# Optimization experiments

Hardware: AMD Instinct MI355X
Metric: run time of the kernel (lower is better)

The kernel has to match this reference:

```python
import jax, jax.numpy as jnp
import numpy as np

DELTA_PULL = 0.5
DELTA_PUSH = 1.5
EPS = 1e-6


def setup_inputs() -> dict:
    key = jax.random.key(0)
    k1, k2 = jax.random.split(key)
    B, C, H, W, K = 4, 16, 512, 512, 16
    embedding_maps = jax.random.normal(k1, (B, C, H, W), dtype=jnp.float32)
    instance_masks = jax.random.randint(k2, (B, K, H, W), 0, 2, dtype=jnp.int32)
    return {"embedding_maps": embedding_maps, "instance_masks": instance_masks}


def reference(embedding_maps, instance_masks):
    emb = embedding_maps                      # [B, C, H, W]
    m = (instance_masks > 0).astype(emb.dtype)  # [B, K, H, W]
    K = m.shape[1]

    # per-instance masked segment reductions over all H*W pixels
    counts = m.sum((-1, -2))                                   # [B, K]
    sums = jnp.einsum('bchw,bkhw->bkc', emb, m)                # [B, K, C]
    sq_sums = jnp.einsum('bchw,bkhw->bkc', emb * emb, m)       # [B, K, C]

    valid = counts > 0                                          # [B, K]
    safe_counts = jnp.maximum(counts, 1.0)
    means = sums / safe_counts[..., None]                       # [B, K, C] exact fg mean

    # sum over fg pixels of ||e - mean||^2 = sq_sum - 2*mean.sum + n*mean^2
    pull_k = (sq_sums - 2.0 * means * sums + counts[..., None] * means * means).sum(-1)
    pull_k = jnp.where(valid, pull_k / (counts + EPS), 0.0)     # [B, K]

    M = valid.sum(-1).astype(emb.dtype)                         # [B] num valid instances
    pull_b = pull_k.sum(-1) / jnp.maximum(M, 1.0)               # [B]

    # pairwise push between valid instance means (i < j)
    diff = means[:, :, None, :] - means[:, None, :, :]          # [B, K, K, C]
    dist = jnp.sqrt((diff * diff).sum(-1) + 1e-12)              # [B, K, K]
    iu = jnp.arange(K)
    pair = valid[:, :, None] & valid[:, None, :] & (iu[:, None] < iu[None, :])
    push_terms = jnp.where(pair, jnp.maximum(DELTA_PUSH - dist, 0.0) ** 2, 0.0)
    npairs = M * (M - 1.0) / 2.0
    push_b = jnp.where(M > 1.0, push_terms.sum((-1, -2)) / jnp.maximum(npairs, 1.0), 0.0)

    return (DELTA_PULL * pull_b + push_b).mean()
```

## Files before the change

### kernel.cpp

```cpp
#include <hip/hip_runtime.h>

#define BB 4
#define CC 16
#define KK 16
#define HWP (512 * 512)
#define THREADS 512
#define TPW 128
#define TPB ((THREADS / 64) * TPW)
#define NTILES (HWP / TPB)
#define NGROUP (TPW / 32)
#define NWAVE (THREADS / 64)
#define NSLICE 16
#define WSTOT (64 + 1024 + 1024)

typedef short bf16x8 __attribute__((ext_vector_type(8)));
typedef float f32x4 __attribute__((ext_vector_type(4)));

__device__ __forceinline__ float fmaxf_(float a, float b) { return a > b ? a : b; }

__device__ __forceinline__ unsigned short f2bf(float f) {
    unsigned u = __float_as_uint(f);
    u += 0x7FFFu + ((u >> 16) & 1u);
    return (unsigned short)(u >> 16);
}
__device__ __forceinline__ unsigned pkbf(float x, float y) {
    return (unsigned)f2bf(x) | ((unsigned)f2bf(y) << 16);
}

__global__ __launch_bounds__(THREADS, 8) void disc_mfma_kernel(
    const float* __restrict__ emb, const int* __restrict__ masks,
    float* __restrict__ ws)
{
    __shared__ __align__(16) unsigned short bits[TPB];
    __shared__ float redbuf[NWAVE][64][9];
    __shared__ float cnt_red[NWAVE][16];

    const int tid = threadIdx.x;
    const int lane = tid & 63;
    const int wave = tid >> 6;
    const int b = blockIdx.x / NTILES;
    const int tile = blockIdx.x % NTILES;
    const size_t base_px = (size_t)tile * TPB + wave * TPW;

    const int quad = lane >> 4;
    const int r = lane & 15;

    const int* mbase = masks + (size_t)b * KK * HWP + base_px + 2 * lane;
    unsigned v0 = 0, v1 = 0;
    #pragma unroll
    for (int k = 0; k < KK; ++k) {
        int2 mm = *(const int2*)(mbase + (size_t)k * HWP);
        v0 |= (mm.x > 0 ? 1u : 0u) << k;
        v1 |= (mm.y > 0 ? 1u : 0u) << k;
    }
    ((unsigned*)bits)[wave * (TPW / 2) + lane] = v0 | (v1 << 16);

    union { bf16x8 v; unsigned short s[8]; } Bones;
    #pragma unroll
    for (int i = 0; i < 8; ++i) Bones.s[i] = 0x3F80;

    const float* ebase = emb + ((size_t)b * CC + r) * HWP + base_px;

    f32x4 acc_s = {0.f, 0.f, 0.f, 0.f};
    f32x4 acc_q = {0.f, 0.f, 0.f, 0.f};
    f32x4 acc_c = {0.f, 0.f, 0.f, 0.f};

    #pragma unroll
    for (int g = 0; g < NGROUP; ++g) {
        const int p0 = wave * TPW + g * 32;

        uint4 bw = *(const uint4*)&bits[p0 + quad * 8];
        union { bf16x8 v; unsigned u[4]; } A;
        A.u[0] = ((bw.x >> r) & 0x00010001u) * 0x3F80u;
        A.u[1] = ((bw.y >> r) & 0x00010001u) * 0x3F80u;
        A.u[2] = ((bw.z >> r) & 0x00010001u) * 0x3F80u;
        A.u[3] = ((bw.w >> r) & 0x00010001u) * 0x3F80u;

        const float4* ep = (const float4*)(ebase + g * 32 + quad * 8);
        float4 f0 = ep[0], f1 = ep[1];
        union { bf16x8 v; unsigned u[4]; } Bf, B2;
        Bf.u[0] = pkbf(f0.x, f0.y);
        Bf.u[1] = pkbf(f0.z, f0.w);
        Bf.u[2] = pkbf(f1.x, f1.y);
        Bf.u[3] = pkbf(f1.z, f1.w);
        B2.u[0] = pkbf(f0.x * f0.x, f0.y * f0.y);
        B2.u[1] = pkbf(f0.z * f0.z, f0.w * f0.w);
        B2.u[2] = pkbf(f1.x * f1.x, f1.y * f1.y);
        B2.u[3] = pkbf(f1.z * f1.z, f1.w * f1.w);

        acc_s = __builtin_amdgcn_mfma_f32_16x16x32_bf16(A.v, Bf.v, acc_s, 0, 0, 0);
        acc_q = __builtin_amdgcn_mfma_f32_16x16x32_bf16(A.v, B2.v, acc_q, 0, 0, 0);
        acc_c = __builtin_amdgcn_mfma_f32_16x16x32_bf16(A.v, Bones.v, acc_c, 0, 0, 0);
    }

    #pragma unroll
    for (int j = 0; j < 4; ++j) {
        redbuf[wave][lane][j] = acc_s[j];
        redbuf[wave][lane][4 + j] = acc_q[j];
    }
    if (r == 0) {
        #pragma unroll
        for (int reg = 0; reg < 4; ++reg) cnt_red[wave][quad * 4 + reg] = acc_c[reg];
    }
    __syncthreads();

    float* slice = ws + (size_t)(blockIdx.x & (NSLICE - 1)) * WSTOT;
    {
        const int fi = tid;
        const int l2 = fi >> 3, j = fi & 7;
        float v = 0.f;
        #pragma unroll
        for (int w = 0; w < NWAVE; ++w) v += redbuf[w][l2][j];
        const int reg = j & 3, isq = j >> 2;
        const int krow = (l2 >> 4) * 4 + reg;
        const int ccol = l2 & 15;
        atomicAdd(&slice[64 + isq * 1024 + ((size_t)b * KK + krow) * CC + ccol], v);
    }
    if (tid < KK) {
        float ctot = 0.f;
        #pragma unroll
        for (int w = 0; w < NWAVE; ++w) ctot += cnt_red[w][tid];
        atomicAdd(&slice[b * KK + tid], ctot);
    }
}

__global__ __launch_bounds__(1024) void disc_finalize_kernel(
    const float* __restrict__ ws, float* __restrict__ out)
{
    __shared__ float red[WSTOT];
    __shared__ float means[BB][KK][CC];
    __shared__ float partial[BB];
    const int tid = threadIdx.x;

    for (int i4 = tid; i4 < WSTOT / 4; i4 += 1024) {
        float4 t = {0.f, 0.f, 0.f, 0.f};
        #pragma unroll
        for (int s = 0; s < NSLICE; ++s) {
            float4 v = *(const float4*)(ws + (size_t)s * WSTOT + 4 * i4);
            t.x += v.x; t.y += v.y; t.z += v.z; t.w += v.w;
        }
        *(float4*)(red + 4 * i4) = t;
    }
    __syncthreads();

    const float* red_cnt = red;
    const float* red_sum = red + 64;
    const float* red_sq  = red + 64 + 1024;

    const int b = tid >> 6;
    const int lane = tid & 63;
    const bool active = tid < 256;

    const float DELTA_PULL = 0.5f;
    const float DELTA_PUSH = 1.5f;
    const float EPS = 1e-6f;

    unsigned long long bal = 0ull;
    float M = 0.f, pull_b = 0.f;

    if (active) {
        float cntk = 0.f;
        bool valid = false;
        float pull_k = 0.f;
        if (lane < KK) {
            int k = lane;
            cntk = red_cnt[b * KK + k];
            valid = cntk > 0.f;
            float safe = fmaxf_(cntk, 1.f);
            float acc_sq = 0.f, acc_ss = 0.f;
            #pragma unroll
            for (int c = 0; c < CC; ++c) {
                float sv = red_sum[(b * KK + k) * CC + c];
                means[b][k][c] = sv / safe;
                acc_sq += red_sq[(b * KK + k) * CC + c];
                acc_ss += sv * sv;
            }
            if (valid) pull_k = (acc_sq - acc_ss / cntk) / (cntk + EPS);
        }

        bal = __ballot(lane < KK && valid);
        M = (float)__popcll(bal);

        float ps = pull_k;
        #pragma unroll
        for (int d = 32; d >= 1; d >>= 1) ps += __shfl_xor(ps, d, 64);
        pull_b = ps / fmaxf_(M, 1.f);
    }

    __syncthreads();

    if (active) {
        float push = 0.f;
        for (int t = lane; t < KK * KK; t += 64) {
            int i = t >> 4, j = t & 15;
            if (i < j && ((bal >> i) & 1ull) && ((bal >> j) & 1ull)) {
                float d2 = 1e-12f;
                #pragma unroll
                for (int c = 0; c < CC; ++c) {
                    float df = means[b][i][c] - means[b][j][c];
                    d2 = fmaf(df, df, d2);
                }
                float dist = sqrtf(d2);
                float h = fmaxf_(DELTA_PUSH - dist, 0.f);
                push += h * h;
            }
        }
        #pragma unroll
        for (int d = 32; d >= 1; d >>= 1) push += __shfl_xor(push, d, 64);

        if (lane == 0) {
            float npairs = M * (M - 1.f) * 0.5f;
            float push_b = (M > 1.f) ? push / fmaxf_(npairs, 1.f) : 0.f;
            partial[b] = DELTA_PULL * pull_b + push_b;
        }
    }
    __syncthreads();
    if (tid == 0) {
        out[0] = (partial[0] + partial[1] + partial[2] + partial[3]) * 0.25f;
    }
}

extern "C" void kernel_launch(void* const* d_in, const int* in_sizes, int n_in,
                              void* d_out, int out_size, void* d_ws, size_t ws_size,
                              hipStream_t stream) {
    const float* emb = (const float*)d_in[0];
    const int* masks = (const int*)d_in[1];
    float* ws = (float*)d_ws;

    hipMemsetAsync(d_ws, 0, NSLICE * WSTOT * sizeof(float), stream);

    dim3 grid(BB * NTILES);
    disc_mfma_kernel<<<grid, THREADS, 0, stream>>>(emb, masks, ws);
    disc_finalize_kernel<<<1, 1024, 0, stream>>>(ws, (float*)d_out);
}
```

Measured before the change: 149.7 us.

## Stage mask and embedding tiles into LDS via global_load_lds with XOR swizzle

Each wave now copies its 128-pixel slice of all 16 mask planes and 16 embedding channels straight from global memory into LDS using global_load_lds, with an XOR swizzle to avoid bank conflicts. It then reads the MFMA operands out of LDS instead of bit-packing the masks through shared memory and loading embeddings directly. The block size drops from 512 to 256 threads, and the reduction loop is changed to cover the full 512-entry redbuf with two iterations per thread. This targets global load efficiency and latency. In exchange it uses much more LDS per block, which may cut occupancy, and it waits on all loads before any compute starts.

```diff
diff --git a/kernel.cpp b/kernel.cpp
--- a/kernel.cpp
+++ b/kernel.cpp
@@ -4,7 +4,7 @@
 #define CC 16
 #define KK 16
 #define HWP (512 * 512)
-#define THREADS 512
+#define THREADS 256
 #define TPW 128
 #define TPB ((THREADS / 64) * TPW)
 #define NTILES (HWP / TPB)
@@ -27,11 +27,18 @@
     return (unsigned)f2bf(x) | ((unsigned)f2bf(y) << 16);
 }
 
-__global__ __launch_bounds__(THREADS, 8) void disc_mfma_kernel(
+__device__ __forceinline__ void gld16(const void* g, void* l) {
+    __builtin_amdgcn_global_load_lds(
+        (const __attribute__((address_space(1))) unsigned*)g,
+        (__attribute__((address_space(3))) unsigned*)l, 16, 0, 0);
+}
+
+__global__ __launch_bounds__(THREADS) void disc_mfma_kernel(
     const float* __restrict__ emb, const int* __restrict__ masks,
     float* __restrict__ ws)
 {
-    __shared__ __align__(16) unsigned short bits[TPB];
+    __shared__ __align__(16) int   mstage[NWAVE][KK][128];
+    __shared__ __align__(16) float estage[NWAVE][CC][128];
     __shared__ float redbuf[NWAVE][64][9];
     __shared__ float cnt_red[NWAVE][16];
 
@@ -45,39 +52,45 @@
     const int quad = lane >> 4;
     const int r = lane & 15;
 
-    const int* mbase = masks + (size_t)b * KK * HWP + base_px + 2 * lane;
-    unsigned v0 = 0, v1 = 0;
-    #pragma unroll
-    for (int k = 0; k < KK; ++k) {
-        int2 mm = *(const int2*)(mbase + (size_t)k * HWP);
-        v0 |= (mm.x > 0 ? 1u : 0u) << k;
-        v1 |= (mm.y > 0 ? 1u : 0u) << k;
-    }
-    ((unsigned*)bits)[wave * (TPW / 2) + lane] = v0 | (v1 << 16);
+    const int l31 = lane & 31;
+    const int khalf = lane >> 5;
+    const int* mplane = masks + (size_t)b * KK * HWP + base_px;
+    const float* eplane = emb + (size_t)b * CC * HWP + base_px;
+    #pragma unroll
+    for (int j = 0; j < 8; ++j) {
+        const int k = 2 * j + khalf;
+        const unsigned soff = (unsigned)((l31 ^ (k & 7)) * 4);
+        gld16(mplane + (size_t)k * HWP + soff, &mstage[wave][2 * j][0]);
+        gld16(eplane + (size_t)k * HWP + soff, &estage[wave][2 * j][0]);
+    }
+
+    asm volatile("s_waitcnt vmcnt(0)" ::: "memory");
+    __builtin_amdgcn_sched_barrier(0);
 
     union { bf16x8 v; unsigned short s[8]; } Bones;
     #pragma unroll
     for (int i = 0; i < 8; ++i) Bones.s[i] = 0x3F80;
-
-    const float* ebase = emb + ((size_t)b * CC + r) * HWP + base_px;
 
     f32x4 acc_s = {0.f, 0.f, 0.f, 0.f};
     f32x4 acc_q = {0.f, 0.f, 0.f, 0.f};
     f32x4 acc_c = {0.f, 0.f, 0.f, 0.f};
 
+    const int rx = r & 7;
+
     #pragma unroll
     for (int g = 0; g < NGROUP; ++g) {
-        const int p0 = wave * TPW + g * 32;
-
-        uint4 bw = *(const uint4*)&bits[p0 + quad * 8];
+        const int cbase = g * 8 + quad * 2;
+
+        int4 ma = *(const int4*)&mstage[wave][r][((cbase + 0) ^ rx) * 4];
+        int4 mb = *(const int4*)&mstage[wave][r][((cbase + 1) ^ rx) * 4];
         union { bf16x8 v; unsigned u[4]; } A;
-        A.u[0] = ((bw.x >> r) & 0x00010001u) * 0x3F80u;
-        A.u[1] = ((bw.y >> r) & 0x00010001u) * 0x3F80u;
-        A.u[2] = ((bw.z >> r) & 0x00010001u) * 0x3F80u;
-        A.u[3] = ((bw.w >> r) & 0x00010001u) * 0x3F80u;
-
-        const float4* ep = (const float4*)(ebase + g * 32 + quad * 8);
-        float4 f0 = ep[0], f1 = ep[1];
+        A.u[0] = (ma.x > 0 ? 0x3F80u : 0u) | (ma.y > 0 ? 0x3F800000u : 0u);
+        A.u[1] = (ma.z > 0 ? 0x3F80u : 0u) | (ma.w > 0 ? 0x3F800000u : 0u);
+        A.u[2] = (mb.x > 0 ? 0x3F80u : 0u) | (mb.y > 0 ? 0x3F800000u : 0u);
+        A.u[3] = (mb.z > 0 ? 0x3F80u : 0u) | (mb.w > 0 ? 0x3F800000u : 0u);
+
+        float4 f0 = *(const float4*)&estage[wave][r][((cbase + 0) ^ rx) * 4];
+        float4 f1 = *(const float4*)&estage[wave][r][((cbase + 1) ^ rx) * 4];
         union { bf16x8 v; unsigned u[4]; } Bf, B2;
         Bf.u[0] = pkbf(f0.x, f0.y);
         Bf.u[1] = pkbf(f0.z, f0.w);
@@ -105,8 +118,9 @@
     __syncthreads();
 
     float* slice = ws + (size_t)(blockIdx.x & (NSLICE - 1)) * WSTOT;
-    {
-        const int fi = tid;
+    #pragma unroll
+    for (int t = 0; t < 2; ++t) {
+        const int fi = tid + t * THREADS;
         const int l2 = fi >> 3, j = fi & 7;
         float v = 0.f;
         #pragma unroll
```

Result: faster. 146.7 us (-2.0%).
